# Kernel tuning notes

Hardware: AMD Instinct MI355X
Metric: run time of the kernel (lower is better)

## Reference

```python
import jax, jax.numpy as jnp
import numpy as np

B, L, D = 2, 2048, 2048
NUM_HEADS = 32
KV_GROUPS = 8
GROUP_SIZE = NUM_HEADS // KV_GROUPS  # 4
HEAD_DIM = D // NUM_HEADS            # 64


def _rope_tables(L, hd):
    # standard RoPE angle tables, duplicated across halves to width hd
    inv_freq = 1.0 / (10000.0 ** (np.arange(0, hd, 2, dtype=np.float32) / hd))
    ang = np.arange(L, dtype=np.float32)[:, None] * inv_freq[None, :]  # [L, hd/2]
    cos = np.concatenate([np.cos(ang), np.cos(ang)], axis=-1)
    sin = np.concatenate([np.sin(ang), np.sin(ang)], axis=-1)
    return jnp.asarray(cos), jnp.asarray(sin)


def setup_inputs() -> dict:
    key = jax.random.key(0)
    ks = jax.random.split(key, 6)
    x = jax.random.normal(ks[0], (B, L, D), dtype=jnp.float32)
    mask = jnp.triu(jnp.ones((L, L), dtype=bool), k=1)  # causal: True above diag
    cos, sin = _rope_tables(L, HEAD_DIM)
    s = 0.02
    Wq = jax.random.normal(ks[1], (D, D), dtype=jnp.float32) * s
    Wk = jax.random.normal(ks[2], (D, KV_GROUPS * HEAD_DIM), dtype=jnp.float32) * s
    Wv = jax.random.normal(ks[3], (D, KV_GROUPS * HEAD_DIM), dtype=jnp.float32) * s
    Wo = jax.random.normal(ks[4], (D, D), dtype=jnp.float32) * s
    bo = jnp.zeros((D,), dtype=jnp.float32)
    return {"x": x, "mask": mask, "cos": cos, "sin": sin,
            "Wq": Wq, "Wk": Wk, "Wv": Wv, "Wo": Wo, "bo": bo}


def _apply_rope(t, cos, sin):
    # t: [B, H, L, hd]
    hd = t.shape[-1]
    t1, t2 = t[..., : hd // 2], t[..., hd // 2:]
    rotated = jnp.concatenate([-t2, t1], axis=-1)
    return t * cos[None, None, :, :] + rotated * sin[None, None, :, :]


def reference(x, mask, cos, sin, Wq, Wk, Wv, Wo, bo):
    Bv, Lv, Dv = x.shape
    hd = HEAD_DIM
    q = (x @ Wq).reshape(Bv, Lv, NUM_HEADS, hd).transpose(0, 2, 1, 3)   # [B,H,L,hd]
    k = (x @ Wk).reshape(Bv, Lv, KV_GROUPS, hd).transpose(0, 2, 1, 3)   # [B,G,L,hd]
    v = (x @ Wv).reshape(Bv, Lv, KV_GROUPS, hd).transpose(0, 2, 1, 3)
    q = _apply_rope(q, cos, sin)
    k = _apply_rope(k, cos, sin)
    k = jnp.repeat(k, GROUP_SIZE, axis=1)  # [B,H,L,hd]
    v = jnp.repeat(v, GROUP_SIZE, axis=1)
    scores = jnp.einsum('bhqd,bhkd->bhqk', q, k) / jnp.sqrt(jnp.float32(hd))
    scores = jnp.where(mask[None, None, :, :], -jnp.inf, scores)
    attn = jax.nn.softmax(scores, axis=-1)
    out = jnp.einsum('bhqk,bhkd->bhqd', attn, v)         # [B,H,L,hd]
    out = out.transpose(0, 2, 1, 3).reshape(Bv, Lv, Dv)  # [B,L,D]
    return out @ Wo + bo
```

## Files before the change

### kernel.cpp

```cpp
#include <hip/hip_runtime.h>
#include <cstdint>

typedef unsigned short UST;
typedef __bf16 v8bf __attribute__((ext_vector_type(8)));
typedef float v4f __attribute__((ext_vector_type(4)));

static __device__ __forceinline__ UST f2b(float f) {
  union { float f; uint32_t u; } c; c.f = f;
  uint32_t u = c.u;
  u += 0x7fffu + ((u >> 16) & 1u);
  return (UST)(u >> 16);
}
static __device__ __forceinline__ float b2f(UST h) {
  union { uint32_t u; float f; } c; c.u = ((uint32_t)h) << 16;
  return c.f;
}
static __device__ __forceinline__ uint32_t cvtpk(float lo, float hi) {
  uint32_t r;
  asm("v_cvt_pk_bf16_f32 %0, %1, %2" : "=v"(r) : "v"(lo), "v"(hi));
  return r;
}
static __device__ __forceinline__ float fexp2(float x) {
  float r;
  asm("v_exp_f32 %0, %1" : "=v"(r) : "v"(x));
  return r;
}
template <int N>
static __device__ __forceinline__ void wait_vm() {
  asm volatile("s_waitcnt vmcnt(%0)" :: "i"(N));
}

static __device__ __forceinline__ void gl_lds16(const UST* g, UST* l) {
  __builtin_amdgcn_global_load_lds(
      (const __attribute__((address_space(1))) void*)g,
      (__attribute__((address_space(3))) void*)l, 16, 0, 0);
}

__global__ __launch_bounds__(256) void k_cast(const float* __restrict__ src,
                                              UST* __restrict__ dst) {
  size_t i = (size_t)blockIdx.x * 256 + threadIdx.x;
  const float4* s4 = reinterpret_cast<const float4*>(src) + 2 * i;
  float4 a = s4[0], b = s4[1];
  union { UST s[8]; uint4 v; } r;
  r.s[0] = f2b(a.x); r.s[1] = f2b(a.y); r.s[2] = f2b(a.z); r.s[3] = f2b(a.w);
  r.s[4] = f2b(b.x); r.s[5] = f2b(b.y); r.s[6] = f2b(b.z); r.s[7] = f2b(b.w);
  reinterpret_cast<uint4*>(dst)[i] = r.v;
}

__global__ __launch_bounds__(256) void k_castT(const float* __restrict__ W,
                                               UST* __restrict__ dst, int N, int K) {
  __shared__ float tile[32][33];
  int nt = blockIdx.x * 32, kt = blockIdx.y * 32;
  int tx = threadIdx.x, ty = threadIdx.y;
#pragma unroll
  for (int r = 0; r < 4; ++r)
    tile[ty + r * 8][tx] = W[(size_t)(kt + ty + r * 8) * N + nt + tx];
  __syncthreads();
#pragma unroll
  for (int r = 0; r < 4; ++r)
    dst[(size_t)(nt + ty + r * 8) * K + kt + tx] = f2b(tile[tx][ty + r * 8]);
}

template <int BM, int BN, int WM, int WN, int NMH, int EPI>
__global__ __launch_bounds__(512, 2) void k_gemm2(const UST* __restrict__ A,
                                                  const UST* __restrict__ Bt,
                                                  void* __restrict__ Cv,
                                                  const float* __restrict__ bias,
                                                  int M, int N, int K, int ntn) {
  constexpr int WMR = BM / WM, WNR = BN / WN;
  constexpr int MF = WMR / 16, NF = WNR / 16, MH = MF / NMH;
  constexpr int CA = BM / 128;
  constexpr int CBF = BN / 128;
  constexpr int BREM = (BN % 128) / 64;
  constexpr int AELEMS = 4 * BM * 32;
  __shared__ __align__(16) UST lds[AELEMS + 4 * BN * 32];

  int tid = threadIdx.x, w = tid >> 6, lane = tid & 63;
  int lr = lane & 15, lg = lane >> 4;
  int wm = w / WN, wn = w % WN;

  int q = (int)gridDim.x >> 3;
  int bid = (int)blockIdx.x;
  int swz = (bid & 7) * q + (bid >> 3);
  int mBlk = (swz / ntn) * BM, nBlk = (swz % ntn) * BN;

  v4f acc[MF][NF];
#pragma unroll
  for (int i = 0; i < MF; ++i)
#pragma unroll
    for (int j = 0; j < NF; ++j) acc[i][j] = (v4f){0.f, 0.f, 0.f, 0.f};

  int srow = tid >> 2;
  int scol = ((tid & 3) ^ ((tid >> 3) & 3)) * 8;
  const UST* Abase = A + (size_t)(mBlk + srow) * K + scol;
  const UST* Bbase = Bt + (size_t)(nBlk + srow) * K + scol;
  int ldsW = w * 512;

  auto stageSlice = [&](int v) {
    int reg = v & 3;
    int koff = (v >> 1) * 64 + (v & 1) * 32;
#pragma unroll
    for (int i = 0; i < CA; ++i)
      gl_lds16(Abase + (size_t)(i * 128) * K + koff,
               &lds[reg * BM * 32 + i * 4096 + ldsW]);
#pragma unroll
    for (int i = 0; i < CBF; ++i)
      gl_lds16(Bbase + (size_t)(i * 128) * K + koff,
               &lds[AELEMS + reg * BN * 32 + i * 4096 + ldsW]);
    if constexpr (BREM) {
      if (w < 4)
        gl_lds16(Bbase + (size_t)(CBF * 128) * K + koff,
                 &lds[AELEMS + reg * BN * 32 + CBF * 4096 + ldsW]);
    }
  };
  auto wait2 = [&]() {
    if constexpr (BREM) {
      if (w < 4) wait_vm<2 * (CA + CBF + 1)>();
      else       wait_vm<2 * (CA + CBF)>();
    } else {
      wait_vm<2 * (CA + CBF)>();
    }
  };
  int rslot = ((lg ^ ((lr >> 1) & 3)) * 8);
  auto ldA = [&](int reg, int f) -> v8bf {
    int row = wm * WMR + f * 16 + lr;
    return *(const v8bf*)&lds[(reg * BM + row) * 32 + rslot];
  };
  auto ldB = [&](int reg, int nf) -> v8bf {
    int row = wn * WNR + nf * 16 + lr;
    return *(const v8bf*)&lds[AELEMS + (reg * BN + row) * 32 + rslot];
  };

  int U = K >> 5;
  stageSlice(0); stageSlice(1); stageSlice(2);
  wait2();
  __builtin_amdgcn_s_barrier();

  auto slice = [&](int u, bool issue, int wkind) {
    int reg = u & 3;
    v8bf bfr[NF];
#pragma unroll
    for (int mh = 0; mh < NMH; ++mh) {
      v8bf afr[MH];
      if (mh == 0) {
#pragma unroll
        for (int nf = 0; nf < NF; ++nf) bfr[nf] = ldB(reg, nf);
      }
#pragma unroll
      for (int f = 0; f < MH; ++f) afr[f] = ldA(reg, mh * MH + f);
      if (mh == 0 && issue) stageSlice(u + 3);
      if (mh == NMH - 1) {
        if (wkind == 1) wait2();
        else if (wkind == 2) wait_vm<0>();
      }
      __builtin_amdgcn_s_barrier();
      __builtin_amdgcn_s_setprio(1);
#pragma unroll
      for (int f = 0; f < MH; ++f)
#pragma unroll
        for (int nf = 0; nf < NF; ++nf)
          acc[mh * MH + f][nf] = __builtin_amdgcn_mfma_f32_16x16x32_bf16(
              afr[f], bfr[nf], acc[mh * MH + f][nf], 0, 0, 0);
      __builtin_amdgcn_s_setprio(0);
      __builtin_amdgcn_s_barrier();
    }
  };

  for (int u = 0; u < U - 3; ++u) slice(u, true, 1);
  slice(U - 3, false, 2);
  slice(U - 2, false, 0);
  slice(U - 1, false, 0);

  int row0 = mBlk + wm * WMR + lg * 4;
  int col0 = nBlk + wn * WNR + lr;
#pragma unroll
  for (int fm = 0; fm < MF; ++fm)
#pragma unroll
    for (int nf = 0; nf < NF; ++nf)
#pragma unroll
      for (int r = 0; r < 4; ++r) {
        int row = row0 + fm * 16 + r;
        int col = col0 + nf * 16;
        if constexpr (EPI == 0) {
          ((UST*)Cv)[(size_t)row * N + col] = f2b(acc[fm][nf][r]);
        } else {
          ((float*)Cv)[(size_t)row * N + col] = acc[fm][nf][r] + bias[col];
        }
      }
}

__global__ __launch_bounds__(256) void k_rope(const UST* __restrict__ qkv,
                                              const float* __restrict__ cosT,
                                              const float* __restrict__ sinT,
                                              UST* __restrict__ qh,
                                              UST* __restrict__ kh) {
  int idx = blockIdx.x * 256 + threadIdx.x;
  int q4 = idx & 3;
  int hh = (idx >> 2) % 40;
  int row = idx / 160;
  int l = row & 2047, b = row >> 11;
  int d0 = q4 * 8;
  int col = (hh < 32) ? hh * 64 : 2048 + (hh - 32) * 64;
  const UST* sp = qkv + (size_t)row * 3072 + col + d0;
  union { uint4 v; UST u[8]; } t1, t2, o1, o2;
  t1.v = *(const uint4*)sp;
  t2.v = *(const uint4*)(sp + 32);
  const float4* cp = (const float4*)&cosT[l * 64 + d0];
  const float4* sn = (const float4*)&sinT[l * 64 + d0];
  float4 ca = cp[0], cb = cp[1], sa = sn[0], sb = sn[1];
  float cc[8] = {ca.x, ca.y, ca.z, ca.w, cb.x, cb.y, cb.z, cb.w};
  float ss[8] = {sa.x, sa.y, sa.z, sa.w, sb.x, sb.y, sb.z, sb.w};
  float scale = (hh < 32) ? 0.125f : 1.f;
#pragma unroll
  for (int j = 0; j < 8; ++j) {
    float a = b2f(t1.u[j]), bb = b2f(t2.u[j]);
    o1.u[j] = f2b((a * cc[j] - bb * ss[j]) * scale);
    o2.u[j] = f2b((bb * cc[j] + a * ss[j]) * scale);
  }
  UST* dst = (hh < 32)
      ? qh + (((size_t)b * 32 + hh) * 2048 + l) * 64 + d0
      : kh + (((size_t)b * 8 + (hh - 32)) * 2048 + l) * 64 + d0;
  *(uint4*)dst = o1.v;
  *(uint4*)(dst + 32) = o2.v;
}

__global__ __launch_bounds__(256) void k_vtrans(const UST* __restrict__ qkv,
                                                UST* __restrict__ vt) {
  __shared__ __align__(16) UST tl[64][72];
  int lt = blockIdx.x, bg = blockIdx.y;
  int b = bg >> 3, g = bg & 7;
  int t = threadIdx.x;
  int li = t >> 2, d0 = (t & 3) * 16;
  const UST* src = qkv + (size_t)(b * 2048 + lt * 64 + li) * 3072 + 2560 + g * 64 + d0;
  *(uint4*)&tl[li][d0] = *(const uint4*)src;
  *(uint4*)&tl[li][d0 + 8] = *(const uint4*)(src + 8);
  __syncthreads();
  int d = t >> 2, l0 = (t & 3) * 16;
  union { UST u[8]; uint4 v; } r0, r1;
#pragma unroll
  for (int e = 0; e < 8; ++e) r0.u[e] = tl[l0 + e][d];
#pragma unroll
  for (int e = 0; e < 8; ++e) r1.u[e] = tl[l0 + 8 + e][d];
  UST* dstp = vt + (size_t)((b * 8 + g) * 64 + d) * 2048 + (size_t)lt * 64 + l0;
  *(uint4*)dstp = r0.v;
  *(uint4*)(dstp + 8) = r1.v;
}

__global__ __launch_bounds__(512, 4) void k_attn(const UST* __restrict__ qh,
                                                 const UST* __restrict__ kh,
                                                 const UST* __restrict__ vt,
                                                 UST* __restrict__ outp) {
  __shared__ __align__(16) UST k_s[128 * 72];
  __shared__ __align__(16) UST v_s[64 * 136];
  __shared__ __align__(16) UST p_s[8][16 * 136];
  int bx = blockIdx.x, h = blockIdx.y, b = blockIdx.z;
  int g = h >> 2;
  int tid = threadIdx.x, w = tid >> 6, lane = tid & 63;
  int lr = lane & 15, lg = lane >> 4;

  int ksr = tid >> 2, ksc = (tid & 3) * 16;
  int vsr = tid >> 3, vsc = (tid & 7) * 16;
  const UST* kbase = kh + ((size_t)(b * 8 + g) * 2048 + ksr) * 64 + ksc;
  const UST* vbase = vt + ((size_t)(b * 8 + g) * 64 + vsr) * 2048 + vsc;
  UST* kdst = &k_s[ksr * 72 + ksc];
  UST* vdst = &v_s[vsr * 136 + vsc];

  for (int half = 0; half < 2; ++half) {
    int qt = half ? (15 - bx) : bx;
    int qbase = qt * 128 + w * 16;

    const UST* qp = qh + ((size_t)(b * 32 + h) * 2048 + qbase + lr) * 64 + lg * 8;
    v8bf qf0 = *(const v8bf*)qp;
    v8bf qf1 = *(const v8bf*)(qp + 32);

    float m = -1e30f, ls = 0.f;
    v4f o[4];
#pragma unroll
    for (int dt = 0; dt < 4; ++dt) o[dt] = (v4f){0.f, 0.f, 0.f, 0.f};

    __syncthreads();
    uint4 pk0 = *(const uint4*)kbase, pk1 = *(const uint4*)(kbase + 8);
    uint4 pv0 = *(const uint4*)vbase, pv1 = *(const uint4*)(vbase + 8);
    *(uint4*)kdst = pk0; *(uint4*)(kdst + 8) = pk1;
    *(uint4*)vdst = pv0; *(uint4*)(vdst + 8) = pv1;

    for (int j = 0; j <= qt; ++j) {
      __syncthreads();
      bool pref = (j < qt);
      if (pref) {
        const UST* kg = kbase + (size_t)(j + 1) * 8192;
        const UST* vg = vbase + (j + 1) * 128;
        pk0 = *(const uint4*)kg; pk1 = *(const uint4*)(kg + 8);
        pv0 = *(const uint4*)vg; pv1 = *(const uint4*)(vg + 8);
      }

      v4f st[8];
      __builtin_amdgcn_s_setprio(1);
#pragma unroll
      for (int kt = 0; kt < 8; ++kt) {
        const UST* kr = &k_s[(kt * 16 + lr) * 72 + lg * 8];
        v8bf kf0 = *(const v8bf*)kr;
        v8bf kf1 = *(const v8bf*)(kr + 32);
        v4f z = (v4f){0.f, 0.f, 0.f, 0.f};
        z = __builtin_amdgcn_mfma_f32_16x16x32_bf16(kf0, qf0, z, 0, 0, 0);
        z = __builtin_amdgcn_mfma_f32_16x16x32_bf16(kf1, qf1, z, 0, 0, 0);
        st[kt] = z;
      }
      __builtin_amdgcn_s_setprio(0);
      if (j == qt) {
        int qg = qbase + lr;
#pragma unroll
        for (int kt = 0; kt < 8; ++kt)
#pragma unroll
          for (int r = 0; r < 4; ++r) {
            int kg2 = j * 128 + kt * 16 + 4 * lg + r;
            if (kg2 > qg) st[kt][r] = -1e30f;
          }
      }

      float t0 = fmaxf(fmaxf(st[0][0], st[0][1]), fmaxf(st[0][2], st[0][3]));
      float t1 = fmaxf(fmaxf(st[1][0], st[1][1]), fmaxf(st[1][2], st[1][3]));
      float t2 = fmaxf(fmaxf(st[2][0], st[2][1]), fmaxf(st[2][2], st[2][3]));
      float t3 = fmaxf(fmaxf(st[3][0], st[3][1]), fmaxf(st[3][2], st[3][3]));
      float t4 = fmaxf(fmaxf(st[4][0], st[4][1]), fmaxf(st[4][2], st[4][3]));
      float t5 = fmaxf(fmaxf(st[5][0], st[5][1]), fmaxf(st[5][2], st[5][3]));
      float t6 = fmaxf(fmaxf(st[6][0], st[6][1]), fmaxf(st[6][2], st[6][3]));
      float t7 = fmaxf(fmaxf(st[7][0], st[7][1]), fmaxf(st[7][2], st[7][3]));
      float mx = fmaxf(fmaxf(fmaxf(t0, t1), fmaxf(t2, t3)),
                       fmaxf(fmaxf(t4, t5), fmaxf(t6, t7)));
      mx = fmaxf(mx, __shfl_xor(mx, 16));
      mx = fmaxf(mx, __shfl_xor(mx, 32));

      if (!__all(mx <= m + 8.f)) {
        float mn = fmaxf(m, mx);
        float al = __expf(m - mn);
        m = mn;
        ls *= al;
#pragma unroll
        for (int r = 0; r < 4; ++r) {
          float ar = __shfl(al, 4 * lg + r);
          o[0][r] *= ar; o[1][r] *= ar; o[2][r] *= ar; o[3][r] *= ar;
        }
      }

      constexpr float LOG2E = 1.44269504f;
      float mlog = m * LOG2E;
      float rs = 0.f;
      UST* pw = &p_s[w][lr * 136 + 4 * lg];
#pragma unroll
      for (int kt = 0; kt < 8; ++kt) {
        float p0 = fexp2(__builtin_fmaf(st[kt][0], LOG2E, -mlog));
        float p1 = fexp2(__builtin_fmaf(st[kt][1], LOG2E, -mlog));
        float p2 = fexp2(__builtin_fmaf(st[kt][2], LOG2E, -mlog));
        float p3 = fexp2(__builtin_fmaf(st[kt][3], LOG2E, -mlog));
        rs += (p0 + p1) + (p2 + p3);
        uint2 q2;
        q2.x = cvtpk(p0, p1);
        q2.y = cvtpk(p2, p3);
        *(uint2*)(pw + kt * 16) = q2;
      }

      __builtin_amdgcn_s_setprio(1);
#pragma unroll
      for (int kk = 0; kk < 4; ++kk) {
        v8bf pa = *(const v8bf*)&p_s[w][lr * 136 + kk * 32 + lg * 8];
#pragma unroll
        for (int dt = 0; dt < 4; ++dt) {
          v8bf vb = *(const v8bf*)&v_s[(dt * 16 + lr) * 136 + kk * 32 + lg * 8];
          o[dt] = __builtin_amdgcn_mfma_f32_16x16x32_bf16(pa, vb, o[dt], 0, 0, 0);
        }
      }
      __builtin_amdgcn_s_setprio(0);

      rs += __shfl_xor(rs, 16);
      rs += __shfl_xor(rs, 32);
      ls += rs;

      __syncthreads();
      if (pref) {
        *(uint4*)kdst = pk0; *(uint4*)(kdst + 8) = pk1;
        *(uint4*)vdst = pv0; *(uint4*)(vdst + 8) = pv1;
      }
    }

    float iv = 1.f / ls;
#pragma unroll
    for (int r = 0; r < 4; ++r) {
      float ivr = __shfl(iv, 4 * lg + r);
      size_t rowb = ((size_t)b * 2048 + qbase + 4 * lg + r) * 2048 + h * 64 + lr;
#pragma unroll
      for (int dt = 0; dt < 4; ++dt)
        outp[rowb + dt * 16] = f2b(o[dt][r] * ivr);
    }
  }
}

extern "C" void kernel_launch(void* const* d_in, const int* in_sizes, int n_in,
                              void* d_out, int out_size, void* d_ws, size_t ws_size,
                              hipStream_t stream) {
  const float* x    = (const float*)d_in[0];
  const float* cosT = (const float*)d_in[2];
  const float* sinT = (const float*)d_in[3];
  const float* Wq   = (const float*)d_in[4];
  const float* Wk   = (const float*)d_in[5];
  const float* Wv   = (const float*)d_in[6];
  const float* Wo   = (const float*)d_in[7];
  const float* bo   = (const float*)d_in[8];
  float* out = (float*)d_out;

  char* ws = (char*)d_ws;
  UST* xb   = (UST*)(ws);
  UST* wcat = (UST*)(ws + 16777216);
  UST* wot  = (UST*)(ws + 29360128);
  UST* qkv  = (UST*)(ws + 37748736);
  UST* qhp  = (UST*)(ws + 62914560);
  UST* khp  = (UST*)(ws + 79691776);
  UST* vtp  = (UST*)(ws + 83886080);
  UST* attn_o = xb;

  k_cast<<<4096, 256, 0, stream>>>(x, xb);
  k_castT<<<dim3(64, 64), dim3(32, 8), 0, stream>>>(Wq, wcat, 2048, 2048);
  k_castT<<<dim3(16, 64), dim3(32, 8), 0, stream>>>(Wk, wcat + (size_t)2048 * 2048, 512, 2048);
  k_castT<<<dim3(16, 64), dim3(32, 8), 0, stream>>>(Wv, wcat + (size_t)2560 * 2048, 512, 2048);
  k_castT<<<dim3(64, 64), dim3(32, 8), 0, stream>>>(Wo, wot, 2048, 2048);

  k_gemm2<256, 192, 2, 4, 2, 0><<<256, 512, 0, stream>>>(xb, wcat, qkv, nullptr,
                                                         4096, 3072, 2048, 16);
  k_rope<<<2560, 256, 0, stream>>>(qkv, cosT, sinT, qhp, khp);
  k_vtrans<<<dim3(32, 16), 256, 0, stream>>>(qkv, vtp);
  k_attn<<<dim3(8, 32, 2), 512, 0, stream>>>(qhp, khp, vtp, attn_o);
  k_gemm2<256, 128, 4, 2, 1, 1><<<256, 512, 0, stream>>>(attn_o, wot, out, bo,
                                                         4096, 2048, 2048, 16);
}
```

Measured before the change: 197.4 us.

## Give each attention wave two 16-row query tiles, halving block size

```diff
diff --git a/kernel.cpp b/kernel.cpp
--- a/kernel.cpp
+++ b/kernel.cpp
@@ -246,20 +246,20 @@
   *(uint4*)(dstp + 8) = r1.v;
 }
 
-__global__ __launch_bounds__(512, 4) void k_attn(const UST* __restrict__ qh,
+__global__ __launch_bounds__(256, 2) void k_attn(const UST* __restrict__ qh,
                                                  const UST* __restrict__ kh,
                                                  const UST* __restrict__ vt,
                                                  UST* __restrict__ outp) {
   __shared__ __align__(16) UST k_s[128 * 72];
   __shared__ __align__(16) UST v_s[64 * 136];
-  __shared__ __align__(16) UST p_s[8][16 * 136];
+  __shared__ __align__(16) UST p_s[4][32 * 136];
   int bx = blockIdx.x, h = blockIdx.y, b = blockIdx.z;
   int g = h >> 2;
   int tid = threadIdx.x, w = tid >> 6, lane = tid & 63;
   int lr = lane & 15, lg = lane >> 4;
 
-  int ksr = tid >> 2, ksc = (tid & 3) * 16;
-  int vsr = tid >> 3, vsc = (tid & 7) * 16;
+  int ksr = tid >> 1, ksc = (tid & 1) * 32;
+  int vsr = tid >> 2, vsc = (tid & 3) * 32;
   const UST* kbase = kh + ((size_t)(b * 8 + g) * 2048 + ksr) * 64 + ksc;
   const UST* vbase = vt + ((size_t)(b * 8 + g) * 64 + vsr) * 2048 + vsc;
   UST* kdst = &k_s[ksr * 72 + ksc];
@@ -267,22 +267,35 @@
 
   for (int half = 0; half < 2; ++half) {
     int qt = half ? (15 - bx) : bx;
-    int qbase = qt * 128 + w * 16;
-
-    const UST* qp = qh + ((size_t)(b * 32 + h) * 2048 + qbase + lr) * 64 + lg * 8;
-    v8bf qf0 = *(const v8bf*)qp;
-    v8bf qf1 = *(const v8bf*)(qp + 32);
-
-    float m = -1e30f, ls = 0.f;
-    v4f o[4];
-#pragma unroll
-    for (int dt = 0; dt < 4; ++dt) o[dt] = (v4f){0.f, 0.f, 0.f, 0.f};
+    int qbase = qt * 128 + w * 32;
+
+    v8bf qf[2][2];
+#pragma unroll
+    for (int mt = 0; mt < 2; ++mt) {
+      const UST* qp = qh + ((size_t)(b * 32 + h) * 2048 + qbase + mt * 16 + lr) * 64 + lg * 8;
+      qf[mt][0] = *(const v8bf*)qp;
+      qf[mt][1] = *(const v8bf*)(qp + 32);
+    }
+
+    float m[2] = {-1e30f, -1e30f}, ls[2] = {0.f, 0.f};
+    v4f o[2][4];
+#pragma unroll
+    for (int mt = 0; mt < 2; ++mt)
+#pragma unroll
+      for (int dt = 0; dt < 4; ++dt) o[mt][dt] = (v4f){0.f, 0.f, 0.f, 0.f};
 
     __syncthreads();
-    uint4 pk0 = *(const uint4*)kbase, pk1 = *(const uint4*)(kbase + 8);
-    uint4 pv0 = *(const uint4*)vbase, pv1 = *(const uint4*)(vbase + 8);
-    *(uint4*)kdst = pk0; *(uint4*)(kdst + 8) = pk1;
-    *(uint4*)vdst = pv0; *(uint4*)(vdst + 8) = pv1;
+    uint4 pk[4], pv[4];
+#pragma unroll
+    for (int e = 0; e < 4; ++e) {
+      pk[e] = *(const uint4*)(kbase + e * 8);
+      pv[e] = *(const uint4*)(vbase + e * 8);
+    }
+#pragma unroll
+    for (int e = 0; e < 4; ++e) {
+      *(uint4*)(kdst + e * 8) = pk[e];
+      *(uint4*)(vdst + e * 8) = pv[e];
+    }
 
     for (int j = 0; j <= qt; ++j) {
       __syncthreads();
@@ -290,107 +303,132 @@
       if (pref) {
         const UST* kg = kbase + (size_t)(j + 1) * 8192;
         const UST* vg = vbase + (j + 1) * 128;
-        pk0 = *(const uint4*)kg; pk1 = *(const uint4*)(kg + 8);
-        pv0 = *(const uint4*)vg; pv1 = *(const uint4*)(vg + 8);
-      }
-
-      v4f st[8];
+#pragma unroll
+        for (int e = 0; e < 4; ++e) {
+          pk[e] = *(const uint4*)(kg + e * 8);
+          pv[e] = *(const uint4*)(vg + e * 8);
+        }
+      }
+
+      v4f st[2][8];
       __builtin_amdgcn_s_setprio(1);
 #pragma unroll
       for (int kt = 0; kt < 8; ++kt) {
         const UST* kr = &k_s[(kt * 16 + lr) * 72 + lg * 8];
         v8bf kf0 = *(const v8bf*)kr;
         v8bf kf1 = *(const v8bf*)(kr + 32);
-        v4f z = (v4f){0.f, 0.f, 0.f, 0.f};
-        z = __builtin_amdgcn_mfma_f32_16x16x32_bf16(kf0, qf0, z, 0, 0, 0);
-        z = __builtin_amdgcn_mfma_f32_16x16x32_bf16(kf1, qf1, z, 0, 0, 0);
-        st[kt] = z;
+#pragma unroll
+        for (int mt = 0; mt < 2; ++mt) {
+          v4f z = (v4f){0.f, 0.f, 0.f, 0.f};
+          z = __builtin_amdgcn_mfma_f32_16x16x32_bf16(kf0, qf[mt][0], z, 0, 0, 0);
+          z = __builtin_amdgcn_mfma_f32_16x16x32_bf16(kf1, qf[mt][1], z, 0, 0, 0);
+          st[mt][kt] = z;
+        }
       }
       __builtin_amdgcn_s_setprio(0);
       if (j == qt) {
-        int qg = qbase + lr;
-#pragma unroll
-        for (int kt = 0; kt < 8; ++kt)
+#pragma unroll
+        for (int mt = 0; mt < 2; ++mt) {
+          int qg = qbase + mt * 16 + lr;
+#pragma unroll
+          for (int kt = 0; kt < 8; ++kt)
+#pragma unroll
+            for (int r = 0; r < 4; ++r) {
+              int kp = j * 128 + kt * 16 + 4 * lg + r;
+              if (kp > qg) st[mt][kt][r] = -1e30f;
+            }
+        }
+      }
+
+      constexpr float LOG2E = 1.44269504f;
+      float rs[2];
+#pragma unroll
+      for (int mt = 0; mt < 2; ++mt) {
+        float t0 = fmaxf(fmaxf(st[mt][0][0], st[mt][0][1]), fmaxf(st[mt][0][2], st[mt][0][3]));
+        float t1 = fmaxf(fmaxf(st[mt][1][0], st[mt][1][1]), fmaxf(st[mt][1][2], st[mt][1][3]));
+        float t2 = fmaxf(fmaxf(st[mt][2][0], st[mt][2][1]), fmaxf(st[mt][2][2], st[mt][2][3]));
+        float t3 = fmaxf(fmaxf(st[mt][3][0], st[mt][3][1]), fmaxf(st[mt][3][2], st[mt][3][3]));
+        float t4 = fmaxf(fmaxf(st[mt][4][0], st[mt][4][1]), fmaxf(st[mt][4][2], st[mt][4][3]));
+        float t5 = fmaxf(fmaxf(st[mt][5][0], st[mt][5][1]), fmaxf(st[mt][5][2], st[mt][5][3]));
+        float t6 = fmaxf(fmaxf(st[mt][6][0], st[mt][6][1]), fmaxf(st[mt][6][2], st[mt][6][3]));
+        float t7 = fmaxf(fmaxf(st[mt][7][0], st[mt][7][1]), fmaxf(st[mt][7][2], st[mt][7][3]));
+        float mx = fmaxf(fmaxf(fmaxf(t0, t1), fmaxf(t2, t3)),
+                         fmaxf(fmaxf(t4, t5), fmaxf(t6, t7)));
+        mx = fmaxf(mx, __shfl_xor(mx, 16));
+        mx = fmaxf(mx, __shfl_xor(mx, 32));
+
+        if (!__all(mx <= m[mt] + 8.f)) {
+          float mn = fmaxf(m[mt], mx);
+          float al = __expf(m[mt] - mn);
+          m[mt] = mn;
+          ls[mt] *= al;
 #pragma unroll
           for (int r = 0; r < 4; ++r) {
-            int kg2 = j * 128 + kt * 16 + 4 * lg + r;
-            if (kg2 > qg) st[kt][r] = -1e30f;
+            float ar = __shfl(al, 4 * lg + r);
+            o[mt][0][r] *= ar; o[mt][1][r] *= ar;
+            o[mt][2][r] *= ar; o[mt][3][r] *= ar;
           }
-      }
-
-      float t0 = fmaxf(fmaxf(st[0][0], st[0][1]), fmaxf(st[0][2], st[0][3]));
-      float t1 = fmaxf(fmaxf(st[1][0], st[1][1]), fmaxf(st[1][2], st[1][3]));
-      float t2 = fmaxf(fmaxf(st[2][0], st[2][1]), fmaxf(st[2][2], st[2][3]));
-      float t3 = fmaxf(fmaxf(st[3][0], st[3][1]), fmaxf(st[3][2], st[3][3]));
-      float t4 = fmaxf(fmaxf(st[4][0], st[4][1]), fmaxf(st[4][2], st[4][3]));
-      float t5 = fmaxf(fmaxf(st[5][0], st[5][1]), fmaxf(st[5][2], st[5][3]));
-      float t6 = fmaxf(fmaxf(st[6][0], st[6][1]), fmaxf(st[6][2], st[6][3]));
-      float t7 = fmaxf(fmaxf(st[7][0], st[7][1]), fmaxf(st[7][2], st[7][3]));
-      float mx = fmaxf(fmaxf(fmaxf(t0, t1), fmaxf(t2, t3)),
-                       fmaxf(fmaxf(t4, t5), fmaxf(t6, t7)));
-      mx = fmaxf(mx, __shfl_xor(mx, 16));
-      mx = fmaxf(mx, __shfl_xor(mx, 32));
-
-      if (!__all(mx <= m + 8.f)) {
-        float mn = fmaxf(m, mx);
-        float al = __expf(m - mn);
-        m = mn;
-        ls *= al;
-#pragma unroll
-        for (int r = 0; r < 4; ++r) {
-          float ar = __shfl(al, 4 * lg + r);
-          o[0][r] *= ar; o[1][r] *= ar; o[2][r] *= ar; o[3][r] *= ar;
-        }
-      }
-
-      constexpr float LOG2E = 1.44269504f;
-      float mlog = m * LOG2E;
-      float rs = 0.f;
-      UST* pw = &p_s[w][lr * 136 + 4 * lg];
-#pragma unroll
-      for (int kt = 0; kt < 8; ++kt) {
-        float p0 = fexp2(__builtin_fmaf(st[kt][0], LOG2E, -mlog));
-        float p1 = fexp2(__builtin_fmaf(st[kt][1], LOG2E, -mlog));
-        float p2 = fexp2(__builtin_fmaf(st[kt][2], LOG2E, -mlog));
-        float p3 = fexp2(__builtin_fmaf(st[kt][3], LOG2E, -mlog));
-        rs += (p0 + p1) + (p2 + p3);
-        uint2 q2;
-        q2.x = cvtpk(p0, p1);
-        q2.y = cvtpk(p2, p3);
-        *(uint2*)(pw + kt * 16) = q2;
+        }
+
+        float mlog = m[mt] * LOG2E;
+        rs[mt] = 0.f;
+        UST* pw = &p_s[w][(mt * 16 + lr) * 136 + 4 * lg];
+#pragma unroll
+        for (int kt = 0; kt < 8; ++kt) {
+          float p0 = fexp2(__builtin_fmaf(st[mt][kt][0], LOG2E, -mlog));
+          float p1 = fexp2(__builtin_fmaf(st[mt][kt][1], LOG2E, -mlog));
+          float p2 = fexp2(__builtin_fmaf(st[mt][kt][2], LOG2E, -mlog));
+          float p3 = fexp2(__builtin_fmaf(st[mt][kt][3], LOG2E, -mlog));
+          rs[mt] += (p0 + p1) + (p2 + p3);
+          uint2 q2;
+          q2.x = cvtpk(p0, p1);
+          q2.y = cvtpk(p2, p3);
+          *(uint2*)(pw + kt * 16) = q2;
+        }
       }
 
       __builtin_amdgcn_s_setprio(1);
 #pragma unroll
       for (int kk = 0; kk < 4; ++kk) {
-        v8bf pa = *(const v8bf*)&p_s[w][lr * 136 + kk * 32 + lg * 8];
+        v8bf pa0 = *(const v8bf*)&p_s[w][lr * 136 + kk * 32 + lg * 8];
+        v8bf pa1 = *(const v8bf*)&p_s[w][(16 + lr) * 136 + kk * 32 + lg * 8];
 #pragma unroll
         for (int dt = 0; dt < 4; ++dt) {
           v8bf vb = *(const v8bf*)&v_s[(dt * 16 + lr) * 136 + kk * 32 + lg * 8];
-          o[dt] = __builtin_amdgcn_mfma_f32_16x16x32_bf16(pa, vb, o[dt], 0, 0, 0);
+          o[0][dt] = __builtin_amdgcn_mfma_f32_16x16x32_bf16(pa0, vb, o[0][dt], 0, 0, 0);
+          o[1][dt] = __builtin_amdgcn_mfma_f32_16x16x32_bf16(pa1, vb, o[1][dt], 0, 0, 0);
         }
       }
       __builtin_amdgcn_s_setprio(0);
 
-      rs += __shfl_xor(rs, 16);
-      rs += __shfl_xor(rs, 32);
-      ls += rs;
+#pragma unroll
+      for (int mt = 0; mt < 2; ++mt) {
+        rs[mt] += __shfl_xor(rs[mt], 16);
+        rs[mt] += __shfl_xor(rs[mt], 32);
+        ls[mt] += rs[mt];
+      }
 
       __syncthreads();
       if (pref) {
-        *(uint4*)kdst = pk0; *(uint4*)(kdst + 8) = pk1;
-        *(uint4*)vdst = pv0; *(uint4*)(vdst + 8) = pv1;
-      }
-    }
-
-    float iv = 1.f / ls;
-#pragma unroll
-    for (int r = 0; r < 4; ++r) {
-      float ivr = __shfl(iv, 4 * lg + r);
-      size_t rowb = ((size_t)b * 2048 + qbase + 4 * lg + r) * 2048 + h * 64 + lr;
-#pragma unroll
-      for (int dt = 0; dt < 4; ++dt)
-        outp[rowb + dt * 16] = f2b(o[dt][r] * ivr);
+#pragma unroll
+        for (int e = 0; e < 4; ++e) {
+          *(uint4*)(kdst + e * 8) = pk[e];
+          *(uint4*)(vdst + e * 8) = pv[e];
+        }
+      }
+    }
+
+#pragma unroll
+    for (int mt = 0; mt < 2; ++mt) {
+      float iv = 1.f / ls[mt];
+#pragma unroll
+      for (int r = 0; r < 4; ++r) {
+        float ivr = __shfl(iv, 4 * lg + r);
+        size_t rowb = ((size_t)b * 2048 + qbase + mt * 16 + 4 * lg + r) * 2048 + h * 64 + lr;
+#pragma unroll
+        for (int dt = 0; dt < 4; ++dt)
+          outp[rowb + dt * 16] = f2b(o[mt][dt][r] * ivr);
+      }
     }
   }
 }
@@ -428,7 +466,7 @@
                                                          4096, 3072, 2048, 16);
   k_rope<<<2560, 256, 0, stream>>>(qkv, cosT, sinT, qhp, khp);
   k_vtrans<<<dim3(32, 16), 256, 0, stream>>>(qkv, vtp);
-  k_attn<<<dim3(8, 32, 2), 512, 0, stream>>>(qhp, khp, vtp, attn_o);
+  k_attn<<<dim3(8, 32, 2), 256, 0, stream>>>(qhp, khp, vtp, attn_o);
   k_gemm2<256, 128, 4, 2, 1, 1><<<256, 512, 0, stream>>>(attn_o, wot, out, bo,
                                                          4096, 2048, 2048, 16);
 }
```

Measured after the change: 248.3 us. 1.26x slower.
